# Kernel tuning notes

Hardware: AMD Instinct MI355X
Metric: run time of the kernel (lower is better)

Reference implementation:

```python
import jax, jax.numpy as jnp
import numpy as np

OBJ = 6
N_OBJS = 16
ACT = 32
HID = 128


def _mlp(x, W1, b1, W2, b2, W3, b3):
    # RoboticsMLP with layer_sizes=[128,128]: Linear->ReLU->Linear->ReLU->Linear
    h = jax.nn.relu(x @ W1 + b1)
    h = jax.nn.relu(h @ W2 + b2)
    return h @ W3 + b3


def setup_inputs() -> dict:
    key = jax.random.key(0)
    ks = jax.random.split(key, 16)
    B = 4096
    s = lambda fan_in: 1.0 / np.sqrt(fan_in)
    u_in = OBJ + ACT          # 38
    b_in = 2 * OBJ + ACT      # 44
    return {
        "config": jax.random.normal(ks[0], (B, N_OBJS * OBJ), dtype=jnp.float32),
        "action": jax.random.normal(ks[1], (B, ACT), dtype=jnp.float32),
        "uW1": jax.random.normal(ks[2], (u_in, HID), dtype=jnp.float32) * s(u_in),
        "ub1": jnp.zeros((HID,), jnp.float32),
        "uW2": jax.random.normal(ks[3], (HID, HID), dtype=jnp.float32) * s(HID),
        "ub2": jnp.zeros((HID,), jnp.float32),
        "uW3": jax.random.normal(ks[4], (HID, OBJ), dtype=jnp.float32) * s(HID),
        "ub3": jnp.zeros((OBJ,), jnp.float32),
        "bW1": jax.random.normal(ks[5], (b_in, HID), dtype=jnp.float32) * s(b_in),
        "bb1": jnp.zeros((HID,), jnp.float32),
        "bW2": jax.random.normal(ks[6], (HID, HID), dtype=jnp.float32) * s(HID),
        "bb2": jnp.zeros((HID,), jnp.float32),
        "bW3": jax.random.normal(ks[7], (HID, OBJ), dtype=jnp.float32) * s(HID),
        "bb3": jnp.zeros((OBJ,), jnp.float32),
    }


def reference(config, action, uW1, ub1, uW2, ub2, uW3, ub3,
              bW1, bb1, bW2, bb2, bW3, bb3):
    B = config.shape[0]
    objs = config.reshape(B, N_OBJS, OBJ)                       # [B, N, 6]

    # Unary: per-object MLP on [obj, action]
    act_b = jnp.broadcast_to(action[:, None, :], (B, N_OBJS, ACT))
    u_in = jnp.concatenate([objs, act_b], axis=-1)              # [B, N, 6+A]
    u_out = _mlp(u_in, uW1, ub1, uW2, ub2, uW3, ub3)            # [B, N, 6]

    # Binary: all ordered pairs (i, j), i != j: [obj_i, obj_j, action]
    oi = jnp.broadcast_to(objs[:, :, None, :], (B, N_OBJS, N_OBJS, OBJ))
    oj = jnp.broadcast_to(objs[:, None, :, :], (B, N_OBJS, N_OBJS, OBJ))
    act_p = jnp.broadcast_to(action[:, None, None, :], (B, N_OBJS, N_OBJS, ACT))
    b_in = jnp.concatenate([oi, oj, act_p], axis=-1)            # [B, N, N, 12+A]
    b_out = _mlp(b_in, bW1, bb1, bW2, bb2, bW3, bb3)            # [B, N, N, 6]

    # zero out diagonal (i == j skipped in original) then sum over j
    mask = (1.0 - jnp.eye(N_OBJS, dtype=b_out.dtype))[None, :, :, None]
    b_sum = (b_out * mask).sum(axis=2)                          # [B, N, 6]

    out = objs + u_out + b_sum
    return out.reshape(B, N_OBJS * OBJ)
```

## Files before the change

kernel.cpp:

```cpp
#include <hip/hip_runtime.h>

typedef short bf16x8 __attribute__((ext_vector_type(8)));
typedef float f32x4 __attribute__((ext_vector_type(4)));

__device__ __forceinline__ unsigned short f2bf(float f) {
    unsigned int u = __float_as_uint(f);
    unsigned int r = u + 0x7FFFu + ((u >> 16) & 1u);
    return (unsigned short)(r >> 16);
}

__device__ __forceinline__ unsigned pkbf(float a, float b) {
    unsigned r;
    asm volatile("v_cvt_pk_bf16_f32 %0, %1, %2" : "=v"(r) : "v"(a), "v"(b));
    return r;
}

__global__ __launch_bounds__(256) void prep_all(
        const float* __restrict__ uW1, const float* __restrict__ uW2, const float* __restrict__ uW3,
        const float* __restrict__ bW1, const float* __restrict__ bW2, const float* __restrict__ bW3,
        unsigned short* __restrict__ ws) {
    int idx = blockIdx.x * 256 + threadIdx.x;
    const float* W; int Ksrc, Nsrc, ntsh; unsigned short* dst; int li;
    if (idx < 8192)       { W = uW1; Ksrc = 38;  Nsrc = 128; ntsh = 10; dst = ws;         li = idx; }
    else if (idx < 16384) { W = bW1; Ksrc = 44;  Nsrc = 128; ntsh = 10; dst = ws + 8192;  li = idx - 8192; }
    else if (idx < 32768) { W = uW2; Ksrc = 128; Nsrc = 128; ntsh = 11; dst = ws + 16384; li = idx - 16384; }
    else if (idx < 49152) { W = bW2; Ksrc = 128; Nsrc = 128; ntsh = 11; dst = ws + 32768; li = idx - 32768; }
    else if (idx < 51200) { W = uW3; Ksrc = 128; Nsrc = 6;   ntsh = 11; dst = ws + 49152; li = idx - 49152; }
    else if (idx < 53248) { W = bW3; Ksrc = 128; Nsrc = 6;   ntsh = 11; dst = ws + 51200; li = idx - 51200; }
    else return;
    int e  = li & 7;
    int l  = (li >> 3) & 63;
    int KS = (ntsh == 10) ? 2 : 4;
    int ks = (li >> 9) & (KS - 1);
    int nt = li >> ntsh;
    int k  = ks * 32 + (l >> 4) * 8 + e;
    int n  = nt * 16 + (l & 15);
    float v = (k < Ksrc && n < Nsrc) ? W[k * Nsrc + n] : 0.0f;
    dst[li] = f2bf(v);
}

__global__ __launch_bounds__(256, 3) void unary_kernel(
        const float* __restrict__ config, const float* __restrict__ action,
        const unsigned short* __restrict__ W1f, const float* __restrict__ b1,
        const unsigned short* __restrict__ W2f, const float* __restrict__ b2,
        const unsigned short* __restrict__ W3f, const float* __restrict__ b3,
        float* __restrict__ out) {
    __shared__ __align__(16) unsigned char smem[4 * 8192];
    const int tid = threadIdx.x;
    const int w = tid >> 6;
    const int l = tid & 63;
    const int g = l >> 4;
    const int c = l & 15;
    unsigned char* buf = smem + w * 8192;

    {
        const int rowL = l >> 1;
        const int kh   = l & 1;
        const int sw   = (rowL & 7) << 4;
        const int base = rowL * 128 + kh * 64;
        const int rg = blockIdx.x * 128 + w * 32 + rowL;
        const int b = rg >> 4;
        const int i = rg & 15;
        const float* cbr = config + b * 96 + i * 6;
        const float* ab  = action + b * 32;
        if (kh == 0) {
            float ov[6];
            { const float2 t0 = *(const float2*)(cbr);
              const float2 t1 = *(const float2*)(cbr + 2);
              const float2 t2 = *(const float2*)(cbr + 4);
              ov[0]=t0.x; ov[1]=t0.y; ov[2]=t1.x; ov[3]=t1.y; ov[4]=t2.x; ov[5]=t2.y; }
            float av[26];
            #pragma unroll
            for (int q = 0; q < 6; ++q) {
                const float4 t = *(const float4*)(ab + 4 * q);
                av[4*q]=t.x; av[4*q+1]=t.y; av[4*q+2]=t.z; av[4*q+3]=t.w;
            }
            { const float2 t = *(const float2*)(ab + 24); av[24]=t.x; av[25]=t.y; }
            #pragma unroll
            for (int ch = 0; ch < 4; ++ch) {
                float x[8];
                #pragma unroll
                for (int t8 = 0; t8 < 8; ++t8) {
                    const int k = ch * 8 + t8;
                    x[t8] = (k < 6) ? ov[k] : av[k - 6];
                }
                union { unsigned uu[4]; bf16x8 v; } U;
                U.uu[0] = pkbf(x[0], x[1]); U.uu[1] = pkbf(x[2], x[3]);
                U.uu[2] = pkbf(x[4], x[5]); U.uu[3] = pkbf(x[6], x[7]);
                *(bf16x8*)(buf + ((base + ch * 16) ^ sw)) = U.v;
            }
        } else {
            float av2[6];
            { const float2 t = *(const float2*)(ab + 26); av2[0]=t.x; av2[1]=t.y; }
            { const float4 t = *(const float4*)(ab + 28); av2[2]=t.x; av2[3]=t.y; av2[4]=t.z; av2[5]=t.w; }
            {
                union { unsigned uu[4]; bf16x8 v; } U;
                U.uu[0] = pkbf(av2[0], av2[1]); U.uu[1] = pkbf(av2[2], av2[3]);
                U.uu[2] = pkbf(av2[4], av2[5]); U.uu[3] = 0u;
                *(bf16x8*)(buf + ((base + 0) ^ sw)) = U.v;
            }
            const bf16x8 z = {0,0,0,0,0,0,0,0};
            *(bf16x8*)(buf + ((base + 16) ^ sw)) = z;
            *(bf16x8*)(buf + ((base + 32) ^ sw)) = z;
            *(bf16x8*)(buf + ((base + 48) ^ sw)) = z;
        }
    }
    __syncthreads();

    const f32x4 zero4 = {0.f, 0.f, 0.f, 0.f};

    bf16x8 xf[2][2];
    #pragma unroll
    for (int mt = 0; mt < 2; ++mt)
        #pragma unroll
        for (int ks = 0; ks < 2; ++ks) {
            const int row = mt * 16 + c;
            xf[mt][ks] = *(const bf16x8*)(buf + ((row * 128 + ks * 64 + g * 16) ^ ((c & 7) << 4)));
        }

    #pragma unroll
    for (int nh = 0; nh < 2; ++nh) {
        f32x4 acc[2][4];
        #pragma unroll
        for (int mt = 0; mt < 2; ++mt)
            #pragma unroll
            for (int ntl = 0; ntl < 4; ++ntl) acc[mt][ntl] = zero4;
        #pragma unroll
        for (int ntl = 0; ntl < 4; ++ntl) {
            const int nt = nh * 4 + ntl;
            #pragma unroll
            for (int ks = 0; ks < 2; ++ks) {
                const bf16x8 bfr = *(const bf16x8*)(W1f + ((nt * 2 + ks) * 64 + l) * 8);
                #pragma unroll
                for (int mt = 0; mt < 2; ++mt)
                    acc[mt][ntl] = __builtin_amdgcn_mfma_f32_16x16x32_bf16(xf[mt][ks], bfr, acc[mt][ntl], 0, 0, 0);
            }
        }
        #pragma unroll
        for (int ntl = 0; ntl < 4; ++ntl) {
            const int col = (nh * 4 + ntl) * 16 + c;
            const float bias = b1[col];
            #pragma unroll
            for (int mt = 0; mt < 2; ++mt)
                #pragma unroll
                for (int r = 0; r < 4; ++r) {
                    const int row = mt * 16 + g * 4 + r;
                    const float hv = fmaxf(acc[mt][ntl][r] + bias, 0.f);
                    *(unsigned short*)(buf + ((row * 256 + col * 2) ^ ((row & 7) << 4))) = f2bf(hv);
                }
        }
    }
    __syncthreads();

    bf16x8 hf[2][4];
    #pragma unroll
    for (int mt = 0; mt < 2; ++mt)
        #pragma unroll
        for (int ks = 0; ks < 4; ++ks) {
            const int row = mt * 16 + c;
            hf[mt][ks] = *(const bf16x8*)(buf + ((row * 256 + ks * 64 + g * 16) ^ ((c & 7) << 4)));
        }

    #pragma unroll
    for (int nh = 0; nh < 2; ++nh) {
        f32x4 acc[2][4];
        #pragma unroll
        for (int mt = 0; mt < 2; ++mt)
            #pragma unroll
            for (int ntl = 0; ntl < 4; ++ntl) acc[mt][ntl] = zero4;
        #pragma unroll
        for (int ntl = 0; ntl < 4; ++ntl) {
            const int nt = nh * 4 + ntl;
            #pragma unroll
            for (int ks = 0; ks < 4; ++ks) {
                const bf16x8 bfr = *(const bf16x8*)(W2f + ((nt * 4 + ks) * 64 + l) * 8);
                #pragma unroll
                for (int mt = 0; mt < 2; ++mt)
                    acc[mt][ntl] = __builtin_amdgcn_mfma_f32_16x16x32_bf16(hf[mt][ks], bfr, acc[mt][ntl], 0, 0, 0);
            }
        }
        #pragma unroll
        for (int ntl = 0; ntl < 4; ++ntl) {
            const int col = (nh * 4 + ntl) * 16 + c;
            const float bias = b2[col];
            #pragma unroll
            for (int mt = 0; mt < 2; ++mt)
                #pragma unroll
                for (int r = 0; r < 4; ++r) {
                    const int row = mt * 16 + g * 4 + r;
                    const float hv = fmaxf(acc[mt][ntl][r] + bias, 0.f);
                    *(unsigned short*)(buf + ((row * 256 + col * 2) ^ ((row & 7) << 4))) = f2bf(hv);
                }
        }
    }
    __syncthreads();

    bf16x8 h2f[2][4];
    #pragma unroll
    for (int mt = 0; mt < 2; ++mt)
        #pragma unroll
        for (int ks = 0; ks < 4; ++ks) {
            const int row = mt * 16 + c;
            h2f[mt][ks] = *(const bf16x8*)(buf + ((row * 256 + ks * 64 + g * 16) ^ ((c & 7) << 4)));
        }

    f32x4 acc3[2];
    acc3[0] = zero4; acc3[1] = zero4;
    #pragma unroll
    for (int ks = 0; ks < 4; ++ks) {
        const bf16x8 bfr = *(const bf16x8*)(W3f + (ks * 64 + l) * 8);
        #pragma unroll
        for (int mt = 0; mt < 2; ++mt)
            acc3[mt] = __builtin_amdgcn_mfma_f32_16x16x32_bf16(h2f[mt][ks], bfr, acc3[mt], 0, 0, 0);
    }

    const int rgbase = blockIdx.x * 128 + w * 32;
    const float b3v = (c < 6) ? b3[c] : 0.f;
    #pragma unroll
    for (int mt = 0; mt < 2; ++mt)
        #pragma unroll
        for (int r = 0; r < 4; ++r) {
            const int rg = rgbase + mt * 16 + g * 4 + r;
            const int b = rg >> 4, i = rg & 15;
            if (c < 6) {
                const int idx = b * 96 + i * 6 + c;
                out[idx] = acc3[mt][r] + b3v + config[idx];
            }
        }
}

__global__ __launch_bounds__(256, 4) void binary_kernel(
        const float* __restrict__ config, const float* __restrict__ action,
        const unsigned short* __restrict__ W1f, const float* __restrict__ b1,
        const unsigned short* __restrict__ W2f, const float* __restrict__ b2,
        const unsigned short* __restrict__ W3f, const float* __restrict__ b3,
        float* __restrict__ out) {
    __shared__ __align__(16) unsigned char Ts[4096];
    __shared__ __align__(16) unsigned char PQs[16384];
    __shared__ __align__(16) unsigned char Cks[8192];

    const int tid = threadIdx.x;
    const int w = tid >> 6, l = tid & 63, g = l >> 4, c = l & 15;
    const int b = blockIdx.x >> 1, h = blockIdx.x & 1;
    const float* cb = config + b * 96;
    const float* ab = action + b * 32;
    const f32x4 zero4 = {0.f, 0.f, 0.f, 0.f};

    {
        const int p  = tid >> 3;
        const int k0 = (tid & 7) * 8;
        union { unsigned short us[8]; bf16x8 v; } u;
        #pragma unroll
        for (int e = 0; e < 8; ++e) {
            const int k = k0 + e;
            float x = 0.f;
            if (p < 16) {
                if (k < 6) x = cb[p * 6 + k];
                else if (k >= 12 && k < 44) x = ab[k - 12];
            } else {
                if (k >= 6 && k < 12) x = cb[(p - 16) * 6 + (k - 6)];
            }
            u.us[e] = f2bf(x);
        }
        *(bf16x8*)(Ts + ((p * 128 + k0 * 2) ^ ((p & 7) << 4))) = u.v;
    }
    __syncthreads();

    {
        bf16x8 tfr[2][2];
        #pragma unroll
        for (int nt = 0; nt < 2; ++nt)
            #pragma unroll
            for (int ks = 0; ks < 2; ++ks)
                tfr[nt][ks] = *(const bf16x8*)(Ts + (((c + 16 * nt) * 128 + 64 * ks + 16 * g) ^ ((c & 7) << 4)));
        f32x4 acc1[2][2];
        acc1[0][0] = zero4; acc1[0][1] = zero4; acc1[1][0] = zero4; acc1[1][1] = zero4;
        #pragma unroll
        for (int mt1 = 0; mt1 < 2; ++mt1) {
            #pragma unroll
            for (int ks = 0; ks < 2; ++ks) {
                const bf16x8 wfr = *(const bf16x8*)(W1f + (((2 * w + mt1) * 2 + ks) * 64 + l) * 8);
                acc1[mt1][0] = __builtin_amdgcn_mfma_f32_16x16x32_bf16(wfr, tfr[0][ks], acc1[mt1][0], 0, 0, 0);
                acc1[mt1][1] = __builtin_amdgcn_mfma_f32_16x16x32_bf16(wfr, tfr[1][ks], acc1[mt1][1], 0, 0, 0);
            }
        }
        #pragma unroll
        for (int mt1 = 0; mt1 < 2; ++mt1) {
            const f32x4 bv = *(const f32x4*)(b1 + 32 * w + 16 * mt1 + 4 * g);
            acc1[mt1][0] = acc1[mt1][0] + bv;
            #pragma unroll
            for (int nt = 0; nt < 2; ++nt) {
                const int p = c + 16 * nt;
                const int fb = (32 * w + 16 * mt1 + 4 * g) * 4;
                float2 v0; v0.x = acc1[mt1][nt][0]; v0.y = acc1[mt1][nt][1];
                float2 v1; v1.x = acc1[mt1][nt][2]; v1.y = acc1[mt1][nt][3];
                *(float2*)(PQs + ((p * 512 + fb)     ^ ((p & 7) << 4))) = v0;
                *(float2*)(PQs + ((p * 512 + fb + 8) ^ ((p & 7) << 4))) = v1;
            }
        }
    }
    __syncthreads();

    const int i0 = h * 8 + 2 * w;
    bf16x8 h1f[2][4];
    #pragma unroll
    for (int nt = 0; nt < 2; ++nt) {
        const int i = i0 + nt;
        #pragma unroll
        for (int ks = 0; ks < 4; ++ks) {
            const int kb = (32 * ks + 8 * g) * 4;
            const f32x4 p0 = *(const f32x4*)(PQs + ((i * 512 + kb) ^ ((i & 7) << 4)));
            const f32x4 p1 = *(const f32x4*)(PQs + ((i * 512 + kb + 16) ^ ((i & 7) << 4)));
            const f32x4 q0 = *(const f32x4*)(PQs + (((16 + c) * 512 + kb) ^ ((c & 7) << 4)));
            const f32x4 q1 = *(const f32x4*)(PQs + (((16 + c) * 512 + kb + 16) ^ ((c & 7) << 4)));
            union { unsigned u[4]; bf16x8 v; } un;
            un.u[0] = pkbf(fmaxf(p0[0] + q0[0], 0.f), fmaxf(p0[1] + q0[1], 0.f));
            un.u[1] = pkbf(fmaxf(p0[2] + q0[2], 0.f), fmaxf(p0[3] + q0[3], 0.f));
            un.u[2] = pkbf(fmaxf(p1[0] + q1[0], 0.f), fmaxf(p1[1] + q1[1], 0.f));
            un.u[3] = pkbf(fmaxf(p1[2] + q1[2], 0.f), fmaxf(p1[3] + q1[3], 0.f));
            h1f[nt][ks] = un.v;
        }
    }

    unsigned char* Ck = Cks + w * 2048;
    f32x4 acc3[2];
    acc3[0] = zero4; acc3[1] = zero4;
    #pragma unroll 1
    for (int ks = 0; ks < 4; ++ks) {
        f32x4 a2[2][2];
        a2[0][0] = zero4; a2[0][1] = zero4; a2[1][0] = zero4; a2[1][1] = zero4;
        #pragma unroll
        for (int ksp = 0; ksp < 4; ++ksp) {
            #pragma unroll
            for (int mt1 = 0; mt1 < 2; ++mt1) {
                const bf16x8 wf = *(const bf16x8*)(W2f + (((2 * ks + mt1) * 4 + ksp) * 64 + l) * 8);
                a2[mt1][0] = __builtin_amdgcn_mfma_f32_16x16x32_bf16(wf, h1f[0][ksp], a2[mt1][0], 0, 0, 0);
                a2[mt1][1] = __builtin_amdgcn_mfma_f32_16x16x32_bf16(wf, h1f[1][ksp], a2[mt1][1], 0, 0, 0);
            }
        }
        #pragma unroll
        for (int mt1 = 0; mt1 < 2; ++mt1) {
            const f32x4 bv = *(const f32x4*)(b2 + 32 * ks + 16 * mt1 + 4 * g);
            #pragma unroll
            for (int nt = 0; nt < 2; ++nt) {
                const int p = c + 16 * nt;
                uint2 pk2;
                pk2.x = pkbf(fmaxf(a2[mt1][nt][0] + bv[0], 0.f), fmaxf(a2[mt1][nt][1] + bv[1], 0.f));
                pk2.y = pkbf(fmaxf(a2[mt1][nt][2] + bv[2], 0.f), fmaxf(a2[mt1][nt][3] + bv[3], 0.f));
                *(uint2*)(Ck + ((p * 64 + 32 * mt1 + 8 * g) ^ (((p >> 1) & 3) << 4))) = pk2;
            }
        }
        const bf16x8 w3 = *(const bf16x8*)(W3f + (ks * 64 + l) * 8);
        #pragma unroll
        for (int nt = 0; nt < 2; ++nt) {
            const int p = c + 16 * nt;
            const bf16x8 ha = *(const bf16x8*)(Ck + ((p * 64 + 16 * g) ^ (((p >> 1) & 3) << 4)));
            acc3[nt] = __builtin_amdgcn_mfma_f32_16x16x32_bf16(ha, w3, acc3[nt], 0, 0, 0);
        }
    }

    const float b3v = (c < 6) ? b3[c] : 0.f;
    #pragma unroll
    for (int nt = 0; nt < 2; ++nt) {
        const int i = i0 + nt;
        float s = 0.f;
        #pragma unroll
        for (int r = 0; r < 4; ++r) {
            const int j = 4 * g + r;
            if (j != i) s += acc3[nt][r] + b3v;
        }
        s += __shfl_xor(s, 16, 64);
        s += __shfl_xor(s, 32, 64);
        if (g == 0 && c < 6) out[b * 96 + i * 6 + c] += s;
    }
}

extern "C" void kernel_launch(void* const* d_in, const int* in_sizes, int n_in,
                              void* d_out, int out_size, void* d_ws, size_t ws_size,
                              hipStream_t stream) {
    const float* config = (const float*)d_in[0];
    const float* action = (const float*)d_in[1];
    const float* uW1 = (const float*)d_in[2];
    const float* ub1 = (const float*)d_in[3];
    const float* uW2 = (const float*)d_in[4];
    const float* ub2 = (const float*)d_in[5];
    const float* uW3 = (const float*)d_in[6];
    const float* ub3 = (const float*)d_in[7];
    const float* bW1 = (const float*)d_in[8];
    const float* bb1 = (const float*)d_in[9];
    const float* bW2 = (const float*)d_in[10];
    const float* bb2 = (const float*)d_in[11];
    const float* bW3 = (const float*)d_in[12];
    const float* bb3 = (const float*)d_in[13];
    float* out = (float*)d_out;

    unsigned short* ws   = (unsigned short*)d_ws;
    unsigned short* uW1f = ws;
    unsigned short* bW1f = ws + 8192;
    unsigned short* uW2f = ws + 16384;
    unsigned short* bW2f = ws + 32768;
    unsigned short* uW3f = ws + 49152;
    unsigned short* bW3f = ws + 51200;

    prep_all<<<208, 256, 0, stream>>>(uW1, uW2, uW3, bW1, bW2, bW3, ws);
    unary_kernel<<<512, 256, 0, stream>>>(config, action, uW1f, ub1, uW2f, ub2, uW3f, ub3, out);
    binary_kernel<<<8192, 256, 0, stream>>>(config, action, bW1f, bb1, bW2f, bb2, bW3f, bb3, out);
}
```

Before: 163.8 us.

## Shrink binary kernel LDS by computing only needed rows and aliasing buffers

Each block now builds first-layer P rows only for the 8 objects i it owns, not all 16, so PQs shrinks from 16 KB to 12 KB. The T staging buffer and the per-wave Ck scratch now share one 8 KB region. Total LDS per block drops from 28 KB to 20 KB, and the launch bound rises to 5 blocks per CU to raise occupancy. The risk is register pressure under the tighter bound, and T must no longer be in use when Ck reuses its memory, which the existing barriers appear to guarantee.

```diff
diff --git a/kernel.cpp b/kernel.cpp
--- a/kernel.cpp
+++ b/kernel.cpp
@@ -229,16 +229,16 @@
         }
 }
 
-__global__ __launch_bounds__(256, 4) void binary_kernel(
+__global__ __launch_bounds__(256, 5) void binary_kernel(
         const float* __restrict__ config, const float* __restrict__ action,
         const unsigned short* __restrict__ W1f, const float* __restrict__ b1,
         const unsigned short* __restrict__ W2f, const float* __restrict__ b2,
         const unsigned short* __restrict__ W3f, const float* __restrict__ b3,
         float* __restrict__ out) {
-    __shared__ __align__(16) unsigned char Ts[4096];
-    __shared__ __align__(16) unsigned char PQs[16384];
-    __shared__ __align__(16) unsigned char Cks[8192];
-
+    __shared__ __align__(16) unsigned char PQs[12288];
+    __shared__ __align__(16) unsigned char UNs[8192];
+
+    unsigned char* Ts = UNs;
     const int tid = threadIdx.x;
     const int w = tid >> 6, l = tid & 63, g = l >> 4, c = l & 15;
     const int b = blockIdx.x >> 1, h = blockIdx.x & 1;
@@ -254,10 +254,10 @@
         for (int e = 0; e < 8; ++e) {
             const int k = k0 + e;
             float x = 0.f;
-            if (p < 16) {
-                if (k < 6) x = cb[p * 6 + k];
+            if (p < 8) {
+                if (k < 6) x = cb[(8 * h + p) * 6 + k];
                 else if (k >= 12 && k < 44) x = ab[k - 12];
-            } else {
+            } else if (p >= 16) {
                 if (k >= 6 && k < 12) x = cb[(p - 16) * 6 + (k - 6)];
             }
             u.us[e] = f2bf(x);
@@ -288,14 +288,19 @@
         for (int mt1 = 0; mt1 < 2; ++mt1) {
             const f32x4 bv = *(const f32x4*)(b1 + 32 * w + 16 * mt1 + 4 * g);
             acc1[mt1][0] = acc1[mt1][0] + bv;
-            #pragma unroll
-            for (int nt = 0; nt < 2; ++nt) {
-                const int p = c + 16 * nt;
-                const int fb = (32 * w + 16 * mt1 + 4 * g) * 4;
-                float2 v0; v0.x = acc1[mt1][nt][0]; v0.y = acc1[mt1][nt][1];
-                float2 v1; v1.x = acc1[mt1][nt][2]; v1.y = acc1[mt1][nt][3];
-                *(float2*)(PQs + ((p * 512 + fb)     ^ ((p & 7) << 4))) = v0;
-                *(float2*)(PQs + ((p * 512 + fb + 8) ^ ((p & 7) << 4))) = v1;
+            const int fb = (32 * w + 16 * mt1 + 4 * g) * 4;
+            if (c < 8) {
+                float2 v0; v0.x = acc1[mt1][0][0]; v0.y = acc1[mt1][0][1];
+                float2 v1; v1.x = acc1[mt1][0][2]; v1.y = acc1[mt1][0][3];
+                *(float2*)(PQs + ((c * 512 + fb)     ^ ((c & 7) << 4))) = v0;
+                *(float2*)(PQs + ((c * 512 + fb + 8) ^ ((c & 7) << 4))) = v1;
+            }
+            {
+                const int row = 8 + c;
+                float2 v0; v0.x = acc1[mt1][1][0]; v0.y = acc1[mt1][1][1];
+                float2 v1; v1.x = acc1[mt1][1][2]; v1.y = acc1[mt1][1][3];
+                *(float2*)(PQs + ((row * 512 + fb)     ^ ((c & 7) << 4))) = v0;
+                *(float2*)(PQs + ((row * 512 + fb + 8) ^ ((c & 7) << 4))) = v1;
             }
         }
     }
@@ -305,14 +310,14 @@
     bf16x8 h1f[2][4];
     #pragma unroll
     for (int nt = 0; nt < 2; ++nt) {
-        const int i = i0 + nt;
+        const int ip = 2 * w + nt;
         #pragma unroll
         for (int ks = 0; ks < 4; ++ks) {
             const int kb = (32 * ks + 8 * g) * 4;
-            const f32x4 p0 = *(const f32x4*)(PQs + ((i * 512 + kb) ^ ((i & 7) << 4)));
-            const f32x4 p1 = *(const f32x4*)(PQs + ((i * 512 + kb + 16) ^ ((i & 7) << 4)));
-            const f32x4 q0 = *(const f32x4*)(PQs + (((16 + c) * 512 + kb) ^ ((c & 7) << 4)));
-            const f32x4 q1 = *(const f32x4*)(PQs + (((16 + c) * 512 + kb + 16) ^ ((c & 7) << 4)));
+            const f32x4 p0 = *(const f32x4*)(PQs + ((ip * 512 + kb) ^ ((ip & 7) << 4)));
+            const f32x4 p1 = *(const f32x4*)(PQs + ((ip * 512 + kb + 16) ^ ((ip & 7) << 4)));
+            const f32x4 q0 = *(const f32x4*)(PQs + (((8 + c) * 512 + kb) ^ ((c & 7) << 4)));
+            const f32x4 q1 = *(const f32x4*)(PQs + (((8 + c) * 512 + kb + 16) ^ ((c & 7) << 4)));
             union { unsigned u[4]; bf16x8 v; } un;
             un.u[0] = pkbf(fmaxf(p0[0] + q0[0], 0.f), fmaxf(p0[1] + q0[1], 0.f));
             un.u[1] = pkbf(fmaxf(p0[2] + q0[2], 0.f), fmaxf(p0[3] + q0[3], 0.f));
@@ -322,7 +327,7 @@
         }
     }
 
-    unsigned char* Ck = Cks + w * 2048;
+    unsigned char* Ck = UNs + w * 2048;
     f32x4 acc3[2];
     acc3[0] = zero4; acc3[1] = zero4;
     #pragma unroll 1
```

Result: no change. 164.3 us (+0.3%).
